# Performance work log

Hardware: AMD Instinct MI355X
Metric: run time of the kernel (lower is better)

Reference implementation:

```python
import jax, jax.numpy as jnp
import numpy as np

HID, OUT = 128, 64
N_SOTU, N_TAXON = 500_000, 200_000
E_TT, E_TS, E_LBL = 200_000, 1_000_000, 500_000


def _sage(x_src, x_dst, src, dst, wl, bl, wr):
    """PyG SAGEConv (mean aggr): lin_l(mean of neighbor msgs) + lin_r(x_dst)."""
    n_dst = x_dst.shape[0]
    agg = jax.ops.segment_sum(x_src[src], dst, num_segments=n_dst)
    deg = jax.ops.segment_sum(jnp.ones(src.shape[0], x_src.dtype), dst, num_segments=n_dst)
    agg = agg / jnp.maximum(deg, 1.0)[:, None]
    return agg @ wl + bl + x_dst @ wr


def setup_inputs() -> dict:
    key = jax.random.key(0)
    ks = iter(jax.random.split(key, 40))

    def w(shape):
        fan_in = shape[0]
        return (jax.random.normal(next(ks), shape, jnp.float32) / np.sqrt(fan_in)).astype(jnp.float32)

    def ri(n, hi):
        return jax.random.randint(next(ks), (n,), 0, hi, dtype=jnp.int32)

    inp = {
        "sotu_ids": jnp.arange(N_SOTU, dtype=jnp.int32),
        "taxon_ids": jnp.arange(N_TAXON, dtype=jnp.int32),
        "ett_src": ri(E_TT, N_TAXON),
        "ett_dst": ri(E_TT, N_TAXON),
        "ets_src": ri(E_TS, N_TAXON),
        "ets_dst": ri(E_TS, N_SOTU),
        "elbl_row": ri(E_LBL, N_SOTU),
        "elbl_col": ri(E_LBL, N_TAXON),
        # embeddings
        "sotu_emb": jax.random.normal(next(ks), (N_SOTU, HID), jnp.float32),
        "taxon_emb": jax.random.normal(next(ks), (N_TAXON, HID), jnp.float32),
        # SOTU encoder: conv1 (taxon->taxon), conv2/3 (taxon->sotu), lin
        "s1_wl": w((HID, HID)), "s1_bl": jnp.zeros((HID,), jnp.float32), "s1_wr": w((HID, HID)),
        "s2_wl": w((HID, HID)), "s2_bl": jnp.zeros((HID,), jnp.float32), "s2_wr": w((HID, HID)),
        "s3_wl": w((HID, HID)), "s3_bl": jnp.zeros((HID,), jnp.float32), "s3_wr": w((HID, HID)),
        "sl_w": w((HID, OUT)), "sl_b": jnp.zeros((OUT,), jnp.float32),
        # Taxon encoder: conv1, conv2, lin
        "t1_wl": w((HID, HID)), "t1_bl": jnp.zeros((HID,), jnp.float32), "t1_wr": w((HID, HID)),
        "t2_wl": w((HID, HID)), "t2_bl": jnp.zeros((HID,), jnp.float32), "t2_wr": w((HID, HID)),
        "tl_w": w((HID, OUT)), "tl_b": jnp.zeros((OUT,), jnp.float32),
        # Edge decoder MLP
        "d1_w": w((2 * OUT, OUT)), "d1_b": jnp.zeros((OUT,), jnp.float32),
        "d2_w": w((OUT, 1)), "d2_b": jnp.zeros((1,), jnp.float32),
    }
    return inp


def reference(sotu_ids, taxon_ids, ett_src, ett_dst, ets_src, ets_dst,
              elbl_row, elbl_col, sotu_emb, taxon_emb,
              s1_wl, s1_bl, s1_wr, s2_wl, s2_bl, s2_wr, s3_wl, s3_bl, s3_wr,
              sl_w, sl_b, t1_wl, t1_bl, t1_wr, t2_wl, t2_bl, t2_wr, tl_w, tl_b,
              d1_w, d1_b, d2_w, d2_b):
    # embedding lookup
    x_sotu = sotu_emb[sotu_ids]          # [N_SOTU, HID]
    x_taxon = taxon_emb[taxon_ids]       # [N_TAXON, HID]
    # SOTU encoder
    taxon_x = jax.nn.relu(_sage(x_taxon, x_taxon, ett_src, ett_dst, s1_wl, s1_bl, s1_wr))
    sotu_x = jax.nn.relu(_sage(x_taxon, x_sotu, ets_src, ets_dst, s2_wl, s2_bl, s2_wr))
    sotu_x = jax.nn.relu(_sage(taxon_x, sotu_x, ets_src, ets_dst, s3_wl, s3_bl, s3_wr))
    z_sotu = sotu_x @ sl_w + sl_b        # [N_SOTU, OUT]
    # Taxon encoder
    tx = jax.nn.relu(_sage(x_taxon, x_taxon, ett_src, ett_dst, t1_wl, t1_bl, t1_wr))
    tx = jax.nn.relu(_sage(tx, tx, ett_src, ett_dst, t2_wl, t2_bl, t2_wr))
    z_taxon = tx @ tl_w + tl_b           # [N_TAXON, OUT]
    # Edge decoder: gather endpoints, fused MLP
    z = jnp.concatenate([z_sotu[elbl_row], z_taxon[elbl_col]], axis=-1)  # [E_LBL, 2*OUT]
    h = jax.nn.relu(z @ d1_w + d1_b)
    return (h @ d2_w + d2_b).reshape(-1)  # [E_LBL]
```

## Files before the change

kernel.cpp:

```cpp
#include <hip/hip_runtime.h>

#define HID 128
#define OUTD 64
#define N_SOTU 500000
#define N_TAXON 200000
#define E_TT 200000
#define E_TS 1000000
#define E_LBL 500000
#define SCAN_TILE 2048

typedef short s16x8 __attribute__((ext_vector_type(8)));
typedef float f32x4 __attribute__((ext_vector_type(4)));

__device__ __forceinline__ unsigned short f2bf(float f) {
    unsigned u = __builtin_bit_cast(unsigned, f);
    u += 0x7FFFu + ((u >> 16) & 1u);
    return (unsigned short)(u >> 16);
}
__device__ __forceinline__ float bf2f(unsigned short h) {
    unsigned u = ((unsigned)h) << 16;
    return __builtin_bit_cast(float, u);
}

__global__ void hist_kernel(const int* __restrict__ dst, int n, int* __restrict__ rp) {
    int e = blockIdx.x * 256 + threadIdx.x;
    if (e < n) atomicAdd(&rp[dst[e]], 1);
}

__global__ __launch_bounds__(256) void scan1_kernel(int* __restrict__ a, int n, int* __restrict__ bsums) {
    __shared__ int tsum[256];
    const int t = threadIdx.x;
    const int base = blockIdx.x * SCAN_TILE + t * 8;
    int v[8]; int s = 0;
#pragma unroll
    for (int i = 0; i < 8; i++) {
        int x = (base + i < n) ? a[base + i] : 0;
        s += x; v[i] = s;
    }
    tsum[t] = s;
    __syncthreads();
    for (int off = 1; off < 256; off <<= 1) {
        int x = (t >= off) ? tsum[t - off] : 0;
        __syncthreads();
        tsum[t] += x;
        __syncthreads();
    }
    const int prev = (t > 0) ? tsum[t - 1] : 0;
#pragma unroll
    for (int i = 0; i < 8; i++)
        if (base + i < n) a[base + i] = v[i] + prev;
    if (t == 255) bsums[blockIdx.x] = tsum[255];
}

__global__ __launch_bounds__(256) void scan2_kernel(int* __restrict__ bsums, int nb) {
    __shared__ int tsum[256];
    const int t = threadIdx.x;
    tsum[t] = (t < nb) ? bsums[t] : 0;
    __syncthreads();
    for (int off = 1; off < 256; off <<= 1) {
        int x = (t >= off) ? tsum[t - off] : 0;
        __syncthreads();
        tsum[t] += x;
        __syncthreads();
    }
    if (t < nb) bsums[t] = tsum[t];
}

__global__ __launch_bounds__(256) void scan3_kernel(int* __restrict__ a, int n, const int* __restrict__ bsums) {
    const int b = blockIdx.x;
    if (b == 0) return;
    const int add = bsums[b - 1];
    const int base = b * SCAN_TILE + threadIdx.x * 8;
#pragma unroll
    for (int i = 0; i < 8; i++)
        if (base + i < n) a[base + i] += add;
}

__global__ void fill_kernel(const int* __restrict__ src, const int* __restrict__ dst, int n,
                            int* __restrict__ rp, int* __restrict__ sl) {
    int e = blockIdx.x * 256 + threadIdx.x;
    if (e < n) {
        int pos = atomicSub(&rp[dst[e]], 1) - 1;
        sl[pos] = src[e];
    }
}

__global__ __launch_bounds__(256) void cvt_kernel(
    int n_rows, const float* __restrict__ xf, const int* __restrict__ ids,
    unsigned short* __restrict__ o)
{
    int idx = blockIdx.x * 256 + threadIdx.x;
    if (idx >= n_rows * 16) return;
    int r = idx >> 4, l = idx & 15;
    int s = ids ? ids[r] : r;
    const float* p = xf + (size_t)s * HID + l * 8;
    float4 v0 = *(const float4*)p;
    float4 v1 = *(const float4*)(p + 4);
    s16x8 ov;
    ov[0] = (short)f2bf(v0.x); ov[1] = (short)f2bf(v0.y);
    ov[2] = (short)f2bf(v0.z); ov[3] = (short)f2bf(v0.w);
    ov[4] = (short)f2bf(v1.x); ov[5] = (short)f2bf(v1.y);
    ov[6] = (short)f2bf(v1.z); ov[7] = (short)f2bf(v1.w);
    *(s16x8*)(o + (size_t)r * HID + l * 8) = ov;
}

__device__ __forceinline__ int wt_idx(int n, int k) {
    return n * 256 + ((((k >> 3) ^ n) & 31) << 3) + (k & 7);
}

__global__ __launch_bounds__(256, 2) void fsage_kernel(
    int n_rows, int row0,
    const unsigned short* __restrict__ gsrc,
    const int* __restrict__ rp, const int* __restrict__ sl,
    int n_dst_total, int n_edges,
    const float* __restrict__ xf, const unsigned short* __restrict__ xb,
    const int* __restrict__ xids,
    const float* __restrict__ wl, const float* __restrict__ wr,
    const float* __restrict__ bl,
    unsigned short* __restrict__ out)
{
    __shared__ __align__(16) unsigned short WT[128 * 256];
    __shared__ __align__(16) unsigned short AGG[4][16 * 128];
    for (int idx = threadIdx.x; idx < 128 * 128; idx += 256) {
        int n = idx & 127, k = idx >> 7;
        WT[wt_idx(n, k)]       = f2bf(wl[idx]);
        WT[wt_idx(n, k + 128)] = f2bf(wr[idx]);
    }
    __syncthreads();
    const int lane = threadIdx.x & 63, wid = threadIdx.x >> 6;
    const int l16 = lane & 15, q = lane >> 4;
    const int n_tiles = n_rows >> 4;
    const int stride = gridDim.x * 4;
    for (int tile = blockIdx.x * 4 + wid; tile < n_tiles; tile += stride) {
        const int base = tile << 4;
        const int lrow = base + l16;
        const size_t xrow = xids ? (size_t)xids[lrow] : (size_t)(row0 + lrow);
        float4 xv[8];
        s16x8 axb[4];
        if (xf) {
            const float* xp = xf + xrow * HID + q * 8;
#pragma unroll
            for (int ks = 0; ks < 4; ++ks) {
                xv[ks * 2]     = *(const float4*)(xp + ks * 32);
                xv[ks * 2 + 1] = *(const float4*)(xp + ks * 32 + 4);
            }
        } else {
            const unsigned short* xp = xb + xrow * HID + q * 8;
#pragma unroll
            for (int ks = 0; ks < 4; ++ks) axb[ks] = *(const s16x8*)(xp + ks * 32);
        }
        int st[4], cc[4];
        s16x8 r[4][4];
        float wgt[4][4];
#pragma unroll
        for (int it = 0; it < 4; ++it) {
            const int lr = it * 4 + q;
            const int d = row0 + base + lr;
            const int s_ = rp[d];
            const int e_ = (d + 1 < n_dst_total) ? rp[d + 1] : n_edges;
            st[it] = s_;
            const int c = e_ - s_;
            cc[it] = c;
            const int js = (s_ < n_edges) ? s_ : (n_edges - 1);
            const int i1 = (c > 1) ? s_ + 1 : js;
            const int i2 = (c > 2) ? s_ + 2 : js;
            const int i3 = (c > 3) ? s_ + 3 : js;
            const int s0 = sl[js], s1 = sl[i1], s2 = sl[i2], s3 = sl[i3];
            r[it][0] = *(const s16x8*)(gsrc + (size_t)s0 * HID + l16 * 8);
            r[it][1] = *(const s16x8*)(gsrc + (size_t)s1 * HID + l16 * 8);
            r[it][2] = *(const s16x8*)(gsrc + (size_t)s2 * HID + l16 * 8);
            r[it][3] = *(const s16x8*)(gsrc + (size_t)s3 * HID + l16 * 8);
            wgt[it][0] = (c > 0) ? 1.0f : 0.0f;
            wgt[it][1] = (c > 1) ? 1.0f : 0.0f;
            wgt[it][2] = (c > 2) ? 1.0f : 0.0f;
            wgt[it][3] = (c > 3) ? 1.0f : 0.0f;
        }
#pragma unroll
        for (int it = 0; it < 4; ++it) {
            float acc[8];
#pragma unroll
            for (int i = 0; i < 8; i++)
                acc[i] = wgt[it][0] * bf2f((unsigned short)r[it][0][i])
                       + wgt[it][1] * bf2f((unsigned short)r[it][1][i])
                       + wgt[it][2] * bf2f((unsigned short)r[it][2][i])
                       + wgt[it][3] * bf2f((unsigned short)r[it][3][i]);
            if (cc[it] > 4) {
                const int e_ = st[it] + cc[it];
                for (int j = st[it] + 4; j < e_; ++j) {
                    const int s = sl[j];
                    s16x8 b = *(const s16x8*)(gsrc + (size_t)s * HID + l16 * 8);
#pragma unroll
                    for (int i = 0; i < 8; i++) acc[i] += bf2f((unsigned short)b[i]);
                }
            }
            const float inv = (cc[it] > 0) ? 1.0f / (float)cc[it] : 0.0f;
            const int lr = it * 4 + q;
            s16x8 o;
#pragma unroll
            for (int i = 0; i < 8; i++) o[i] = (short)f2bf(acc[i] * inv);
            *(s16x8*)&AGG[wid][lr * 128 + ((l16 * 8) ^ ((lr & 7) << 3))] = o;
        }
        asm volatile("s_waitcnt lgkmcnt(0)" ::: "memory");
        s16x8 ax[4];
        if (xf) {
#pragma unroll
            for (int ks = 0; ks < 4; ++ks) {
                float4 v0 = xv[ks * 2], v1 = xv[ks * 2 + 1];
                ax[ks][0] = (short)f2bf(v0.x); ax[ks][1] = (short)f2bf(v0.y);
                ax[ks][2] = (short)f2bf(v0.z); ax[ks][3] = (short)f2bf(v0.w);
                ax[ks][4] = (short)f2bf(v1.x); ax[ks][5] = (short)f2bf(v1.y);
                ax[ks][6] = (short)f2bf(v1.z); ax[ks][7] = (short)f2bf(v1.w);
            }
        } else {
#pragma unroll
            for (int ks = 0; ks < 4; ++ks) ax[ks] = axb[ks];
        }
        f32x4 acc4[8] = {};
#pragma unroll
        for (int ks = 0; ks < 4; ks++) {
            const int cu = ks * 32 + q * 8;
            s16x8 a = *(const s16x8*)&AGG[wid][l16 * 128 + (cu ^ ((l16 & 7) << 3))];
#pragma unroll
            for (int nt = 0; nt < 8; nt++) {
                s16x8 b = *(const s16x8*)&WT[wt_idx(nt * 16 + l16, cu)];
                acc4[nt] = __builtin_amdgcn_mfma_f32_16x16x32_bf16(a, b, acc4[nt], 0, 0, 0);
            }
        }
#pragma unroll
        for (int ks = 0; ks < 4; ks++) {
            const int kb = 128 + ks * 32 + q * 8;
#pragma unroll
            for (int nt = 0; nt < 8; nt++) {
                s16x8 b = *(const s16x8*)&WT[wt_idx(nt * 16 + l16, kb)];
                acc4[nt] = __builtin_amdgcn_mfma_f32_16x16x32_bf16(ax[ks], b, acc4[nt], 0, 0, 0);
            }
        }
#pragma unroll
        for (int nt = 0; nt < 8; nt++) {
            const int n = nt * 16 + l16;
            const float bv = bl[n];
#pragma unroll
            for (int i = 0; i < 4; i++) {
                float v = acc4[nt][i] + bv;
                out[(size_t)(base + q * 4 + i) * HID + n] = f2bf(fmaxf(v, 0.0f));
            }
        }
    }
}

__global__ __launch_bounds__(256) void proj_kernel(
    int n_nodes, const unsigned short* __restrict__ x,
    const float* __restrict__ w, const float* __restrict__ bias, unsigned short* __restrict__ z)
{
    const int lane = threadIdx.x & 63, wid = threadIdx.x >> 6;
    const int l16 = lane & 15, q = lane >> 4;
    s16x8 bfr[4][4];
#pragma unroll
    for (int ks = 0; ks < 4; ks++)
#pragma unroll
        for (int nt = 0; nt < 4; nt++)
#pragma unroll
            for (int i = 0; i < 8; i++)
                bfr[ks][nt][i] = (short)f2bf(w[(ks * 32 + q * 8 + i) * OUTD + nt * 16 + l16]);
    const int n_tiles = n_nodes >> 4;
    const int stride = gridDim.x * 4;
    for (int tile = blockIdx.x * 4 + wid; tile < n_tiles; tile += stride) {
        const int base = tile << 4;
        const size_t mrow = (size_t)(base + l16);
        f32x4 acc[4] = {};
#pragma unroll
        for (int ks = 0; ks < 4; ks++) {
            s16x8 a = *(const s16x8*)(x + mrow * HID + ks * 32 + q * 8);
#pragma unroll
            for (int nt = 0; nt < 4; nt++)
                acc[nt] = __builtin_amdgcn_mfma_f32_16x16x32_bf16(a, bfr[ks][nt], acc[nt], 0, 0, 0);
        }
#pragma unroll
        for (int nt = 0; nt < 4; nt++) {
            const int n = nt * 16 + l16;
            const float bv = bias[n];
#pragma unroll
            for (int i = 0; i < 4; i++)
                z[(size_t)(base + q * 4 + i) * OUTD + n] = f2bf(acc[nt][i] + bv);
        }
    }
}

__global__ __launch_bounds__(256) void dec_kernel(
    const int* __restrict__ erow, const int* __restrict__ ecol,
    const unsigned short* __restrict__ zs, const unsigned short* __restrict__ zt,
    const float* __restrict__ w1, const float* __restrict__ b1,
    const float* __restrict__ w2, const float* __restrict__ b2,
    float* __restrict__ out)
{
    const int lane = threadIdx.x & 63, wid = threadIdx.x >> 6;
    const int l16 = lane & 15, q = lane >> 4;
    s16x8 bfr[4][4];
#pragma unroll
    for (int ks = 0; ks < 4; ks++)
#pragma unroll
        for (int nt = 0; nt < 4; nt++)
#pragma unroll
            for (int i = 0; i < 8; i++)
                bfr[ks][nt][i] = (short)f2bf(w1[(ks * 32 + q * 8 + i) * OUTD + nt * 16 + l16]);
    float b1v[4], w2v[4];
#pragma unroll
    for (int nt = 0; nt < 4; nt++) {
        b1v[nt] = b1[nt * 16 + l16];
        w2v[nt] = w2[nt * 16 + l16];
    }
    const float b2v = b2[0];
    const int n_tiles = E_LBL >> 4;
    for (int tile = blockIdx.x * 4 + wid; tile < n_tiles; tile += gridDim.x * 4) {
        const int em = tile * 16 + l16;
        const size_t r = (size_t)erow[em], c = (size_t)ecol[em];
        f32x4 acc[4] = {};
        s16x8 a0 = *(const s16x8*)(zs + r * OUTD + q * 8);
        s16x8 a1 = *(const s16x8*)(zs + r * OUTD + 32 + q * 8);
        s16x8 a2 = *(const s16x8*)(zt + c * OUTD + q * 8);
        s16x8 a3 = *(const s16x8*)(zt + c * OUTD + 32 + q * 8);
#pragma unroll
        for (int nt = 0; nt < 4; nt++) {
            acc[nt] = __builtin_amdgcn_mfma_f32_16x16x32_bf16(a0, bfr[0][nt], acc[nt], 0, 0, 0);
            acc[nt] = __builtin_amdgcn_mfma_f32_16x16x32_bf16(a1, bfr[1][nt], acc[nt], 0, 0, 0);
            acc[nt] = __builtin_amdgcn_mfma_f32_16x16x32_bf16(a2, bfr[2][nt], acc[nt], 0, 0, 0);
            acc[nt] = __builtin_amdgcn_mfma_f32_16x16x32_bf16(a3, bfr[3][nt], acc[nt], 0, 0, 0);
        }
        float s[4] = {0.0f, 0.0f, 0.0f, 0.0f};
#pragma unroll
        for (int nt = 0; nt < 4; nt++)
#pragma unroll
            for (int i = 0; i < 4; i++)
                s[i] += fmaxf(acc[nt][i] + b1v[nt], 0.0f) * w2v[nt];
#pragma unroll
        for (int off = 8; off >= 1; off >>= 1)
#pragma unroll
            for (int i = 0; i < 4; i++)
                s[i] += __shfl_down(s[i], off, 16);
        if (l16 == 0) {
#pragma unroll
            for (int i = 0; i < 4; i++)
                out[tile * 16 + q * 4 + i] = s[i] + b2v;
        }
    }
}

static void build_csr(const int* src, const int* dst, int n_edges, int n_dst,
                      int* rp, int* sl, int* bsums, hipStream_t stream) {
    hipMemsetAsync(rp, 0, (size_t)n_dst * 4, stream);
    hist_kernel<<<(n_edges + 255) / 256, 256, 0, stream>>>(dst, n_edges, rp);
    const int nb = (n_dst + SCAN_TILE - 1) / SCAN_TILE;
    scan1_kernel<<<nb, 256, 0, stream>>>(rp, n_dst, bsums);
    scan2_kernel<<<1, 256, 0, stream>>>(bsums, nb);
    scan3_kernel<<<nb, 256, 0, stream>>>(rp, n_dst, bsums);
    fill_kernel<<<(n_edges + 255) / 256, 256, 0, stream>>>(src, dst, n_edges, rp, sl);
}

extern "C" void kernel_launch(void* const* d_in, const int* in_sizes, int n_in,
                              void* d_out, int out_size, void* d_ws, size_t ws_size,
                              hipStream_t stream) {
    (void)in_sizes; (void)n_in; (void)out_size; (void)ws_size;
    const int* sotu_ids  = (const int*)d_in[0];
    const int* taxon_ids = (const int*)d_in[1];
    const int* ett_src   = (const int*)d_in[2];
    const int* ett_dst   = (const int*)d_in[3];
    const int* ets_src   = (const int*)d_in[4];
    const int* ets_dst   = (const int*)d_in[5];
    const int* elbl_row  = (const int*)d_in[6];
    const int* elbl_col  = (const int*)d_in[7];
    const float* sotu_emb  = (const float*)d_in[8];
    const float* taxon_emb = (const float*)d_in[9];
    const float* s1_wl = (const float*)d_in[10]; const float* s1_bl = (const float*)d_in[11]; const float* s1_wr = (const float*)d_in[12];
    const float* s2_wl = (const float*)d_in[13]; const float* s2_bl = (const float*)d_in[14]; const float* s2_wr = (const float*)d_in[15];
    const float* s3_wl = (const float*)d_in[16]; const float* s3_bl = (const float*)d_in[17]; const float* s3_wr = (const float*)d_in[18];
    const float* sl_w  = (const float*)d_in[19]; const float* sl_b  = (const float*)d_in[20];
    const float* t1_wl = (const float*)d_in[21]; const float* t1_bl = (const float*)d_in[22]; const float* t1_wr = (const float*)d_in[23];
    const float* t2_wl = (const float*)d_in[24]; const float* t2_bl = (const float*)d_in[25]; const float* t2_wr = (const float*)d_in[26];
    const float* tl_w  = (const float*)d_in[27]; const float* tl_b  = (const float*)d_in[28];
    const float* d1_w  = (const float*)d_in[29]; const float* d1_b  = (const float*)d_in[30];
    const float* d2_w  = (const float*)d_in[31]; const float* d2_b  = (const float*)d_in[32];
    float* out = (float*)d_out;

    char* ws = (char*)d_ws;
    size_t off = 0;
    auto alloc = [&](size_t bytes) { void* p = ws + off; off = (off + bytes + 255) & ~(size_t)255; return p; };
    unsigned short* tb      = (unsigned short*)alloc((size_t)N_TAXON * HID * 2);
    unsigned short* taxon_x = (unsigned short*)alloc((size_t)N_TAXON * HID * 2);
    unsigned short* tx1     = (unsigned short*)alloc((size_t)N_TAXON * HID * 2);
    unsigned short* tx2     = (unsigned short*)alloc((size_t)N_TAXON * HID * 2);
    unsigned short* sotu_x  = (unsigned short*)alloc((size_t)N_SOTU * HID * 2);
    unsigned short* z_taxon = (unsigned short*)alloc((size_t)N_TAXON * OUTD * 2);
    int* rp_ts = (int*)alloc((size_t)N_SOTU * 4);
    int* sl_ts = (int*)alloc((size_t)E_TS * 4);
    int* rp_tt = (int*)alloc((size_t)N_TAXON * 4);
    int* sl_tt = (int*)alloc((size_t)E_TT * 4);
    int* bsums = (int*)alloc(256 * 4);
    unsigned short* z_sotu = tx1;

    build_csr(ett_src, ett_dst, E_TT, N_TAXON, rp_tt, sl_tt, bsums, stream);
    build_csr(ets_src, ets_dst, E_TS, N_SOTU, rp_ts, sl_ts, bsums, stream);

    cvt_kernel<<<(N_TAXON * 16 + 255) / 256, 256, 0, stream>>>(N_TAXON, taxon_emb, taxon_ids, tb);

    fsage_kernel<<<512, 256, 0, stream>>>(N_TAXON, 0, tb, rp_tt, sl_tt, N_TAXON, E_TT,
                                          nullptr, tb, nullptr, s1_wl, s1_wr, s1_bl, taxon_x);
    fsage_kernel<<<512, 256, 0, stream>>>(N_TAXON, 0, tb, rp_tt, sl_tt, N_TAXON, E_TT,
                                          nullptr, tb, nullptr, t1_wl, t1_wr, t1_bl, tx1);

    fsage_kernel<<<512, 256, 0, stream>>>(N_TAXON, 0, tx1, rp_tt, sl_tt, N_TAXON, E_TT,
                                          nullptr, tx1, nullptr, t2_wl, t2_wr, t2_bl, tx2);
    proj_kernel<<<1024, 256, 0, stream>>>(N_TAXON, tx2, tl_w, tl_b, z_taxon);

    fsage_kernel<<<512, 256, 0, stream>>>(N_SOTU, 0, tb, rp_ts, sl_ts, N_SOTU, E_TS,
                                          sotu_emb, nullptr, sotu_ids, s2_wl, s2_wr, s2_bl, sotu_x);
    fsage_kernel<<<512, 256, 0, stream>>>(N_SOTU, 0, taxon_x, rp_ts, sl_ts, N_SOTU, E_TS,
                                          nullptr, sotu_x, nullptr, s3_wl, s3_wr, s3_bl, sotu_x);
    proj_kernel<<<1024, 256, 0, stream>>>(N_SOTU, sotu_x, sl_w, sl_b, z_sotu);

    dec_kernel<<<1024, 256, 0, stream>>>(elbl_row, elbl_col, z_sotu, z_taxon,
                                         d1_w, d1_b, d2_w, d2_b, out);
}
```

Baseline: 1.341 ms.

## Gather first four neighbor rows via global_load_lds into LDS for aggregation

The first four neighbor rows per destination are now fetched straight into shared memory with global_load_lds DMA, using swizzled offsets. Each lane then reduces its own row's features from LDS into MFMA A-operand layout, so the separate AGG round-trip is no longer needed. The tail loop for high-degree rows now runs per lane, wave-uniformly via __any. LDS use grows from 16KB to 64KB per block, so the occupancy hint is dropped and the grid is halved to 256 blocks, which risks lower latency hiding.

Result: slower. 1.377 ms (+2.7%).

```diff
diff --git a/kernel.cpp b/kernel.cpp
--- a/kernel.cpp
+++ b/kernel.cpp
@@ -20,6 +20,12 @@
 __device__ __forceinline__ float bf2f(unsigned short h) {
     unsigned u = ((unsigned)h) << 16;
     return __builtin_bit_cast(float, u);
+}
+
+__device__ __forceinline__ void gload_lds16(const unsigned short* g, unsigned short* l) {
+    __builtin_amdgcn_global_load_lds(
+        (const __attribute__((address_space(1))) unsigned int*)g,
+        (__attribute__((address_space(3))) unsigned int*)l, 16, 0, 0);
 }
 
 __global__ void hist_kernel(const int* __restrict__ dst, int n, int* __restrict__ rp) {
@@ -108,7 +114,7 @@
     return n * 256 + ((((k >> 3) ^ n) & 31) << 3) + (k & 7);
 }
 
-__global__ __launch_bounds__(256, 2) void fsage_kernel(
+__global__ __launch_bounds__(256) void fsage_kernel(
     int n_rows, int row0,
     const unsigned short* __restrict__ gsrc,
     const int* __restrict__ rp, const int* __restrict__ sl,
@@ -120,7 +126,7 @@
     unsigned short* __restrict__ out)
 {
     __shared__ __align__(16) unsigned short WT[128 * 256];
-    __shared__ __align__(16) unsigned short AGG[4][16 * 128];
+    __shared__ __align__(16) unsigned short G[4][16][512];
     for (int idx = threadIdx.x; idx < 128 * 128; idx += 256) {
         int n = idx & 127, k = idx >> 7;
         WT[wt_idx(n, k)]       = f2bf(wl[idx]);
@@ -133,10 +139,11 @@
     const int stride = gridDim.x * 4;
     for (int tile = blockIdx.x * 4 + wid; tile < n_tiles; tile += stride) {
         const int base = tile << 4;
+        const int d0 = row0 + base;
         const int lrow = base + l16;
         const size_t xrow = xids ? (size_t)xids[lrow] : (size_t)(row0 + lrow);
         float4 xv[8];
-        s16x8 axb[4];
+        s16x8 ax[4];
         if (xf) {
             const float* xp = xf + xrow * HID + q * 8;
 #pragma unroll
@@ -147,61 +154,69 @@
         } else {
             const unsigned short* xp = xb + xrow * HID + q * 8;
 #pragma unroll
-            for (int ks = 0; ks < 4; ++ks) axb[ks] = *(const s16x8*)(xp + ks * 32);
-        }
-        int st[4], cc[4];
-        s16x8 r[4][4];
-        float wgt[4][4];
-#pragma unroll
-        for (int it = 0; it < 4; ++it) {
-            const int lr = it * 4 + q;
-            const int d = row0 + base + lr;
-            const int s_ = rp[d];
-            const int e_ = (d + 1 < n_dst_total) ? rp[d + 1] : n_edges;
-            st[it] = s_;
-            const int c = e_ - s_;
-            cc[it] = c;
-            const int js = (s_ < n_edges) ? s_ : (n_edges - 1);
-            const int i1 = (c > 1) ? s_ + 1 : js;
-            const int i2 = (c > 2) ? s_ + 2 : js;
-            const int i3 = (c > 3) ? s_ + 3 : js;
-            const int s0 = sl[js], s1 = sl[i1], s2 = sl[i2], s3 = sl[i3];
-            r[it][0] = *(const s16x8*)(gsrc + (size_t)s0 * HID + l16 * 8);
-            r[it][1] = *(const s16x8*)(gsrc + (size_t)s1 * HID + l16 * 8);
-            r[it][2] = *(const s16x8*)(gsrc + (size_t)s2 * HID + l16 * 8);
-            r[it][3] = *(const s16x8*)(gsrc + (size_t)s3 * HID + l16 * 8);
-            wgt[it][0] = (c > 0) ? 1.0f : 0.0f;
-            wgt[it][1] = (c > 1) ? 1.0f : 0.0f;
-            wgt[it][2] = (c > 2) ? 1.0f : 0.0f;
-            wgt[it][3] = (c > 3) ? 1.0f : 0.0f;
-        }
-#pragma unroll
-        for (int it = 0; it < 4; ++it) {
-            float acc[8];
-#pragma unroll
-            for (int i = 0; i < 8; i++)
-                acc[i] = wgt[it][0] * bf2f((unsigned short)r[it][0][i])
-                       + wgt[it][1] * bf2f((unsigned short)r[it][1][i])
-                       + wgt[it][2] * bf2f((unsigned short)r[it][2][i])
-                       + wgt[it][3] * bf2f((unsigned short)r[it][3][i]);
-            if (cc[it] > 4) {
-                const int e_ = st[it] + cc[it];
-                for (int j = st[it] + 4; j < e_; ++j) {
-                    const int s = sl[j];
-                    s16x8 b = *(const s16x8*)(gsrc + (size_t)s * HID + l16 * 8);
-#pragma unroll
-                    for (int i = 0; i < 8; i++) acc[i] += bf2f((unsigned short)b[i]);
+            for (int ks = 0; ks < 4; ++ks) ax[ks] = *(const s16x8*)(xp + ks * 32);
+        }
+        int sA[4], dA[4];
+#pragma unroll
+        for (int b = 0; b < 4; ++b) {
+            const int r = d0 + 4 * b + q;
+            const int s_ = rp[r];
+            const int e_ = (r + 1 < n_dst_total) ? rp[r + 1] : n_edges;
+            sA[b] = s_; dA[b] = e_ - s_;
+        }
+        const int st16 = rp[d0 + l16];
+        const int e16 = (d0 + l16 + 1 < n_dst_total) ? rp[d0 + l16 + 1] : n_edges;
+        const int d16 = e16 - st16;
+#pragma unroll
+        for (int b = 0; b < 4; ++b) {
+            const int swz = l16 ^ ((4 * b + q) & 7);
+#pragma unroll
+            for (int s = 0; s < 4; ++s) {
+                const int offc = (dA[b] > 0) ? ((s < dA[b]) ? s : (dA[b] - 1)) : 0;
+                int idx = sA[b] + offc;
+                idx = (idx < n_edges) ? idx : (n_edges - 1);
+                const int sv = sl[idx];
+                gload_lds16(gsrc + (size_t)sv * HID + swz * 8, &G[wid][b * 4 + s][0]);
+            }
+        }
+        asm volatile("s_waitcnt vmcnt(0)" ::: "memory");
+        float acc8[4][8];
+#pragma unroll
+        for (int ks = 0; ks < 4; ++ks)
+#pragma unroll
+            for (int i = 0; i < 8; ++i) acc8[ks][i] = 0.0f;
+        const int gi = (l16 >> 2) * 4;
+        const int ro = (l16 & 3) * 128;
+#pragma unroll
+        for (int s = 0; s < 4; ++s) {
+            const float w = (s < d16) ? 1.0f : 0.0f;
+#pragma unroll
+            for (int ks = 0; ks < 4; ++ks) {
+                const int c = (ks * 4 + q) ^ (l16 & 7);
+                s16x8 v = *(const s16x8*)&G[wid][gi + s][ro + c * 8];
+#pragma unroll
+                for (int i = 0; i < 8; ++i) acc8[ks][i] += w * bf2f((unsigned short)v[i]);
+            }
+        }
+        if (__any(d16 > 4)) {
+            for (int j = 4; __any(j < d16); ++j) {
+                if (j < d16) {
+                    const int sv = sl[st16 + j];
+#pragma unroll
+                    for (int ks = 0; ks < 4; ++ks) {
+                        s16x8 v = *(const s16x8*)(gsrc + (size_t)sv * HID + (ks * 4 + q) * 8);
+#pragma unroll
+                        for (int i = 0; i < 8; ++i) acc8[ks][i] += bf2f((unsigned short)v[i]);
+                    }
                 }
             }
-            const float inv = (cc[it] > 0) ? 1.0f / (float)cc[it] : 0.0f;
-            const int lr = it * 4 + q;
-            s16x8 o;
-#pragma unroll
-            for (int i = 0; i < 8; i++) o[i] = (short)f2bf(acc[i] * inv);
-            *(s16x8*)&AGG[wid][lr * 128 + ((l16 * 8) ^ ((lr & 7) << 3))] = o;
-        }
-        asm volatile("s_waitcnt lgkmcnt(0)" ::: "memory");
-        s16x8 ax[4];
+        }
+        const float inv = (d16 > 0) ? 1.0f / (float)d16 : 0.0f;
+        s16x8 aagg[4];
+#pragma unroll
+        for (int ks = 0; ks < 4; ++ks)
+#pragma unroll
+            for (int i = 0; i < 8; ++i) aagg[ks][i] = (short)f2bf(acc8[ks][i] * inv);
         if (xf) {
 #pragma unroll
             for (int ks = 0; ks < 4; ++ks) {
@@ -211,19 +226,15 @@
                 ax[ks][4] = (short)f2bf(v1.x); ax[ks][5] = (short)f2bf(v1.y);
                 ax[ks][6] = (short)f2bf(v1.z); ax[ks][7] = (short)f2bf(v1.w);
             }
-        } else {
-#pragma unroll
-            for (int ks = 0; ks < 4; ++ks) ax[ks] = axb[ks];
         }
         f32x4 acc4[8] = {};
 #pragma unroll
         for (int ks = 0; ks < 4; ks++) {
             const int cu = ks * 32 + q * 8;
-            s16x8 a = *(const s16x8*)&AGG[wid][l16 * 128 + (cu ^ ((l16 & 7) << 3))];
 #pragma unroll
             for (int nt = 0; nt < 8; nt++) {
                 s16x8 b = *(const s16x8*)&WT[wt_idx(nt * 16 + l16, cu)];
-                acc4[nt] = __builtin_amdgcn_mfma_f32_16x16x32_bf16(a, b, acc4[nt], 0, 0, 0);
+                acc4[nt] = __builtin_amdgcn_mfma_f32_16x16x32_bf16(aagg[ks], b, acc4[nt], 0, 0, 0);
             }
         }
 #pragma unroll
@@ -402,18 +413,18 @@
 
     cvt_kernel<<<(N_TAXON * 16 + 255) / 256, 256, 0, stream>>>(N_TAXON, taxon_emb, taxon_ids, tb);
 
-    fsage_kernel<<<512, 256, 0, stream>>>(N_TAXON, 0, tb, rp_tt, sl_tt, N_TAXON, E_TT,
+    fsage_kernel<<<256, 256, 0, stream>>>(N_TAXON, 0, tb, rp_tt, sl_tt, N_TAXON, E_TT,
                                           nullptr, tb, nullptr, s1_wl, s1_wr, s1_bl, taxon_x);
-    fsage_kernel<<<512, 256, 0, stream>>>(N_TAXON, 0, tb, rp_tt, sl_tt, N_TAXON, E_TT,
+    fsage_kernel<<<256, 256, 0, stream>>>(N_TAXON, 0, tb, rp_tt, sl_tt, N_TAXON, E_TT,
                                           nullptr, tb, nullptr, t1_wl, t1_wr, t1_bl, tx1);
 
-    fsage_kernel<<<512, 256, 0, stream>>>(N_TAXON, 0, tx1, rp_tt, sl_tt, N_TAXON, E_TT,
+    fsage_kernel<<<256, 256, 0, stream>>>(N_TAXON, 0, tx1, rp_tt, sl_tt, N_TAXON, E_TT,
                                           nullptr, tx1, nullptr, t2_wl, t2_wr, t2_bl, tx2);
     proj_kernel<<<1024, 256, 0, stream>>>(N_TAXON, tx2, tl_w, tl_b, z_taxon);
 
-    fsage_kernel<<<512, 256, 0, stream>>>(N_SOTU, 0, tb, rp_ts, sl_ts, N_SOTU, E_TS,
+    fsage_kernel<<<256, 256, 0, stream>>>(N_SOTU, 0, tb, rp_ts, sl_ts, N_SOTU, E_TS,
                                           sotu_emb, nullptr, sotu_ids, s2_wl, s2_wr, s2_bl, sotu_x);
-    fsage_kernel<<<512, 256, 0, stream>>>(N_SOTU, 0, taxon_x, rp_ts, sl_ts, N_SOTU, E_TS,
+    fsage_kernel<<<256, 256, 0, stream>>>(N_SOTU, 0, taxon_x, rp_ts, sl_ts, N_SOTU, E_TS,
                                           nullptr, sotu_x, nullptr, s3_wl, s3_wr, s3_bl, sotu_x);
     proj_kernel<<<1024, 256, 0, stream>>>(N_SOTU, sotu_x, sl_w, sl_b, z_sotu);
 
```
